# Kernel tuning notes

Measured on AMD Instinct MI355X. Metric: run time of the kernel, lower is better.

## Reference

```python
import jax, jax.numpy as jnp
import numpy as np
from jax import lax

S, B, I, H, L, O, T = 128, 64, 1024, 1024, 2, 1024, 64


def lstm_cell(x, h, c, wih, whh, b):
    # PyTorch gate order: i, f, g, o
    g = x @ wih.T + h @ whh.T + b  # [B, 4H]
    i, f, gg, o = jnp.split(g, 4, axis=-1)
    c = jax.nn.sigmoid(f) * c + jax.nn.sigmoid(i) * jnp.tanh(gg)
    h = jax.nn.sigmoid(o) * jnp.tanh(c)
    return h, c


def run_lstm_seq(xs, wih, whh, b):
    # xs: [S, B, in]; zero initial state (torch default)
    h0 = jnp.zeros((xs.shape[1], whh.shape[-1]), xs.dtype)

    def step(carry, x):
        h, c = lstm_cell(x, carry[0], carry[1], wih, whh, b)
        return (h, c), h

    (h, c), ys = lax.scan(step, (h0, h0), xs)
    return ys, h, c


def setup_inputs() -> dict:
    key = jax.random.key(0)
    ks = jax.random.split(key, 10)
    s = 1.0 / np.sqrt(H)
    u = lambda k, shape: jax.random.uniform(k, shape, minval=-s, maxval=s, dtype=jnp.float32)
    return {
        "input_seq": jax.random.normal(ks[0], (S, B, I), dtype=jnp.float32),
        "enc_wih": u(ks[1], (L, 4 * H, I)),
        "enc_whh": u(ks[2], (L, 4 * H, H)),
        "enc_b": u(ks[3], (L, 4 * H)),
        "dec_wih": u(ks[4], (L, 4 * H, I)),
        "dec_whh": u(ks[5], (L, 4 * H, H)),
        "dec_b": u(ks[6], (L, 4 * H)),
        "lin_w": u(ks[7], (O, H)),
        "lin_b": u(ks[8], (O,)),
        "target_seq_length": T,
    }


def reference(input_seq, enc_wih, enc_whh, enc_b, dec_wih, dec_whh, dec_b, lin_w, lin_b, target_seq_length):
    # ---- encoder: stacked LSTM over the full sequence ----
    xs = input_seq
    hs, cs = [], []
    for l in range(L):
        xs, h, c = run_lstm_seq(xs, enc_wih[l], enc_whh[l], enc_b[l])
        hs.append(h)
        cs.append(c)
    hs = jnp.stack(hs)  # [L, B, H]
    cs = jnp.stack(cs)

    x0 = input_seq[-1]  # [B, I]

    def dec_step(carry, _):
        x, hs, cs = carry
        inp = x
        nh, nc = [], []
        for l in range(L):
            h, c = lstm_cell(inp, hs[l], cs[l], dec_wih[l], dec_whh[l], dec_b[l])
            nh.append(h)
            nc.append(c)
            inp = h
        y = inp @ lin_w.T + lin_b  # [B, O]
        return (y, jnp.stack(nh), jnp.stack(nc)), y

    _, outs = lax.scan(dec_step, (x0, hs, cs), None, length=target_seq_length)
    return jnp.transpose(outs, (1, 0, 2))  # [B, T, O]
```

## Files before the change

### kernel.cpp

```cpp
#include <hip/hip_runtime.h>
#include <math.h>


typedef unsigned short u16;
typedef short short8 __attribute__((ext_vector_type(8)));
typedef float f32x4 __attribute__((ext_vector_type(4)));

#define MFMA_BF16 __builtin_amdgcn_mfma_f32_16x16x32_bf16

__device__ __forceinline__ u16 f2bf(float x) {
  unsigned u = __builtin_bit_cast(unsigned, x);
  unsigned r = u + 0x7fffu + ((u >> 16) & 1u);
  return (u16)(r >> 16);
}
__device__ __forceinline__ float bf2f(u16 b) {
  return __builtin_bit_cast(float, ((unsigned)b) << 16);
}
__device__ __forceinline__ int permrow(int r) {
  int gate = r >> 10, hc = r & 1023;
  return ((hc >> 2) << 4) + ((hc & 3) << 2) + gate;
}

__device__ __forceinline__ void st_sc(u16* p, u16 v) {
  unsigned vv = v;
  asm volatile("global_store_short %0, %1, off sc0 sc1" :: "v"(p), "v"(vv) : "memory");
}
__device__ __forceinline__ int coh_load(const int* p) {
  int v;
  asm volatile("global_load_dword %0, %1, off sc0 sc1\n\ts_waitcnt vmcnt(0)"
               : "=v"(v) : "v"(p) : "memory");
  return v;
}
__device__ __forceinline__ void coh_store(int* p, int v) {
  asm volatile("global_store_dword %0, %1, off sc0 sc1\n\ts_waitcnt vmcnt(0)"
               :: "v"(p), "v"(v) : "memory");
}


__global__ void split_mat(const float* __restrict__ src, u16* __restrict__ dh,
                          u16* __restrict__ dl, int n, int mode) {
  int i = blockIdx.x * 256 + threadIdx.x;
  if (i >= n) return;
  float v = src[i];
  u16 hi = f2bf(v);
  u16 lo = f2bf(v - bf2f(hi));
  int r = i >> 10, c = i & 1023;
  int idx = i;
  if (mode == 1) idx = c * 1024 + r;
  else if (mode == 2) idx = permrow(r) * 1024 + c;
  dh[idx] = hi; dl[idx] = lo;
}

__global__ void zero_f4(float4* __restrict__ p, int n) {
  int i = blockIdx.x * 256 + threadIdx.x;
  if (i < n) p[i] = make_float4(0.f, 0.f, 0.f, 0.f);
}

__global__ void bias_perm(const float* __restrict__ in, float* __restrict__ out) {
  int i = blockIdx.x * 256 + threadIdx.x;
  if (i < 4096) out[permrow(i)] = in[i];
}

__global__ void bias_comb(const float* __restrict__ db0, const float* __restrict__ lb,
                          const float* __restrict__ wih, float* __restrict__ out) {
  __shared__ float red[256];
  int n = blockIdx.x;
  float s = 0.f;
  for (int k = threadIdx.x; k < 1024; k += 256) s += lb[k] * wih[(size_t)n * 1024 + k];
  red[threadIdx.x] = s;
  __syncthreads();
  for (int d = 128; d > 0; d >>= 1) {
    if (threadIdx.x < d) red[threadIdx.x] += red[threadIdx.x + d];
    __syncthreads();
  }
  if (threadIdx.x == 0) out[permrow(n)] = db0[n] + red[0];
}

template<int MT>
__global__ __launch_bounds__(256) void gemm_split(
    const u16* __restrict__ Ah, const u16* __restrict__ Al, int lda,
    const u16* __restrict__ Bh, const u16* __restrict__ Bl, int ldb,
    int K, int gn,
    u16* __restrict__ Ch, u16* __restrict__ Cl, int ldc,
    float* __restrict__ outp, const float* __restrict__ bias, int ldout, int mode) {
  int bm = blockIdx.x / gn, bn = blockIdx.x % gn;
  int l = threadIdx.x & 63, w = threadIdx.x >> 6;
  int n0 = bn * 128 + w * 32;
  int rr = l & 15, ko = (l >> 4) << 3, q = l >> 4;
  int M0 = bm * 64 * MT;
  f32x4 acc[8 * MT] = {};
  for (int kk = 0; kk < K; kk += 32) {
    short8 bh[2], bl[2];
#pragma unroll
    for (int nt = 0; nt < 2; ++nt) {
      size_t bo = (size_t)(n0 + nt * 16 + rr) * ldb + kk + ko;
      bh[nt] = *(const short8*)(Bh + bo);
      bl[nt] = *(const short8*)(Bl + bo);
    }
#pragma unroll
    for (int mt = 0; mt < 4 * MT; ++mt) {
      size_t ao = (size_t)(M0 + mt * 16 + rr) * lda + kk + ko;
      short8 ah = *(const short8*)(Ah + ao);
      short8 al = *(const short8*)(Al + ao);
#pragma unroll
      for (int nt = 0; nt < 2; ++nt) {
        f32x4 t = acc[mt * 2 + nt];
        t = MFMA_BF16(ah, bh[nt], t, 0, 0, 0);
        t = MFMA_BF16(ah, bl[nt], t, 0, 0, 0);
        t = MFMA_BF16(al, bh[nt], t, 0, 0, 0);
        acc[mt * 2 + nt] = t;
      }
    }
  }
#pragma unroll
  for (int mt = 0; mt < 4 * MT; ++mt)
#pragma unroll
    for (int nt = 0; nt < 2; ++nt)
#pragma unroll
      for (int r = 0; r < 4; ++r) {
        int row = M0 + mt * 16 + q * 4 + r;
        int col = n0 + nt * 16 + rr;
        float v = acc[mt * 2 + nt][r];
        if (mode == 0) {
          u16 hh = f2bf(v);
          Ch[(size_t)row * ldc + col] = hh;
          Cl[(size_t)row * ldc + col] = f2bf(v - bf2f(hh));
        } else if (mode == 1) {
          int t = row >> 6, b = row & 63;
          outp[(size_t)b * 65536 + t * 1024 + col] = v + bias[col];
        } else {
          outp[(size_t)row * ldout + col] = v;
        }
      }
}


struct Half {
  const u16 *Ah, *Al, *Wh, *Wl;
  const float* pre;
  const float* bias;
  float* c;
  u16 *Hh, *Hl;
  int active;
};

__global__ __launch_bounds__(512, 1) void lstm_pair(Half hA, Half hB) {
  int j = blockIdx.x;
  Half S = (j < 128) ? hA : hB;
  if (!S.active) return;
  int sub = j & 127;
  int rowblk = ((sub & 7) << 4) | (sub >> 3);
  int R = rowblk << 5;
  int tid = threadIdx.x;
  int l = tid & 63, w = tid >> 6;
  int rr = l & 15, ko = (l >> 4) << 3, q = l >> 4;
  int kb = w << 7;
  const u16* __restrict__ Wh = S.Wh + (size_t)(R + rr) * 1024 + kb + ko;
  const u16* __restrict__ Wl = S.Wl + (size_t)(R + rr) * 1024 + kb + ko;
  const u16* __restrict__ Ah = S.Ah + kb + ko;
  const u16* __restrict__ Al = S.Al + kb + ko;

  f32x4 acc[8] = {};
#pragma unroll
  for (int kk = 0; kk < 128; kk += 32) {
    short8 bh[2], bl[2];
#pragma unroll
    for (int nt = 0; nt < 2; ++nt) {
      bh[nt] = *(const short8*)(Wh + (size_t)(nt << 4) * 1024 + kk);
      bl[nt] = *(const short8*)(Wl + (size_t)(nt << 4) * 1024 + kk);
    }
#pragma unroll
    for (int mt = 0; mt < 4; ++mt) {
      size_t ao = (size_t)((mt << 4) + rr) * 1024 + kk;
      short8 ah = *(const short8*)(Ah + ao);
      short8 al = *(const short8*)(Al + ao);
#pragma unroll
      for (int nt = 0; nt < 2; ++nt) {
        f32x4 t = acc[mt * 2 + nt];
        t = MFMA_BF16(ah, bh[nt], t, 0, 0, 0);
        t = MFMA_BF16(ah, bl[nt], t, 0, 0, 0);
        t = MFMA_BF16(al, bh[nt], t, 0, 0, 0);
        acc[mt * 2 + nt] = t;
      }
    }
  }

  __shared__ float lds[8][64][33];
#pragma unroll
  for (int mt = 0; mt < 4; ++mt)
#pragma unroll
    for (int nt = 0; nt < 2; ++nt)
#pragma unroll
      for (int r = 0; r < 4; ++r)
        lds[w][(mt << 4) + (q << 2) + r][(nt << 4) + rr] = acc[mt * 2 + nt][r];
  __syncthreads();

  int b = tid >> 3, e = tid & 7;
  float g[4];
#pragma unroll
  for (int gt = 0; gt < 4; ++gt) {
    int c = (e << 2) + gt;
    float s = S.bias[R + c] + S.pre[(size_t)b * 4096 + R + c];
#pragma unroll
    for (int ww = 0; ww < 8; ++ww) s += lds[ww][b][c];
    g[gt] = s;
  }
  int hc = (rowblk << 3) + e;
  size_t ci = (size_t)b * 1024 + hc;
  float cold = S.c[ci];
  float is = 1.f / (1.f + expf(-g[0]));
  float fs = 1.f / (1.f + expf(-g[1]));
  float gg = tanhf(g[2]);
  float os = 1.f / (1.f + expf(-g[3]));
  float cn = fs * cold + is * gg;
  S.c[ci] = cn;
  float h = os * tanhf(cn);
  S.Hh[ci] = f2bf(h);
  S.Hl[ci] = f2bf(h - bf2f(f2bf(h)));
}


struct DecP {
  const u16 *Wch, *Wcl;
  const u16 *W0h, *W0l;
  const u16 *Wi1h, *Wi1l;
  const u16 *Wh1h, *Wh1l;
  const u16 *h0i_h, *h0i_l;
  const u16 *h1i_h, *h1i_l;
  const u16 *zh, *zl;
  const float *Gd0, *dbp0, *bdec0, *dbp1;
  const float *c0, *c1;
  u16 *D0h, *D0l;
  u16 *H1h, *H1l;
  int* bar;
};

__device__ __forceinline__ void gridbar(int* arrive, int* go, int seq, int j) {
  __syncthreads();
  int tid = threadIdx.x;
  if (j == 0) {
    if (tid >= 1 && tid < 256) {
      while (coh_load(arrive + tid) < seq) __builtin_amdgcn_s_sleep(1);
    }
    __syncthreads();
    if (tid == 0) coh_store(go, seq);
  } else {
    if (tid == 0) {
      coh_store(arrive + j, seq);
      while (coh_load(go) < seq) __builtin_amdgcn_s_sleep(1);
    }
  }
  __syncthreads();
}

__global__ __launch_bounds__(512, 1) void lstm_dec_persist(DecP D) {
  int j = blockIdx.x;
  int rowblk = ((j & 7) << 5) | (j >> 3);
  int R = rowblk << 4;
  int tid = threadIdx.x;
  int l = tid & 63, w = tid >> 6;
  int rr = l & 15, ko = (l >> 4) << 3, q = l >> 4;
  int opidx = w >> 2;
  int kb = (w & 3) << 8;
  size_t woff = (size_t)(R + rr) * 1024 + kb + ko;
  int* arrive = D.bar;
  int* go = D.bar + 256;

  const u16* pWAh = (opidx == 0 ? D.Wch : D.W0h) + woff;
  const u16* pWAl = (opidx == 0 ? D.Wcl : D.W0l) + woff;
  const u16* pWBh = (opidx == 0 ? D.Wi1h : D.Wh1h) + woff;
  const u16* pWBl = (opidx == 0 ? D.Wi1l : D.Wh1l) + woff;
  short8 wAh[8], wAl[8], wBh[8], wBl[8];
#pragma unroll
  for (int ki = 0; ki < 8; ++ki) {
    wAh[ki] = *(const short8*)(pWAh + (ki << 5));
    wAl[ki] = *(const short8*)(pWAl + (ki << 5));
    wBh[ki] = *(const short8*)(pWBh + (ki << 5));
    wBl[ki] = *(const short8*)(pWBl + (ki << 5));
  }

  float creg0 = 0.f, creg1 = 0.f;
  float bA[4], bB[4], gb0[4];
  size_t ci = 0;
  if (tid < 256) {
    int b = tid >> 2, e = tid & 3;
    int hc = (rowblk << 2) + e;
    ci = (size_t)b * 1024 + hc;
    creg0 = D.c0[ci];
    creg1 = D.c1[ci];
#pragma unroll
    for (int gt = 0; gt < 4; ++gt) {
      int cc = R + (e << 2) + gt;
      bA[gt] = D.bdec0[cc];
      bB[gt] = D.dbp1[cc];
      gb0[gt] = D.dbp0[cc] + D.Gd0[(size_t)(tid >> 2) * 4096 + cc];
    }
  }

  __shared__ float lds[8][64][17];
  const u16 *h0p_h = D.h0i_h, *h0p_l = D.h0i_l;
  int seq = 0;

  for (int t = 0; t < 64; ++t) {
    u16* d0c_h = D.D0h + (size_t)t * 65536;
    u16* d0c_l = D.D0l + (size_t)t * 65536;
    const u16* h1p_h = (t == 0) ? D.h1i_h : D.H1h + (size_t)(t - 1) * 65536;
    const u16* h1p_l = (t == 0) ? D.h1i_l : D.H1l + (size_t)(t - 1) * 65536;

    {
      const u16* Aph = (opidx == 0) ? (t == 0 ? D.zh : h1p_h) : h0p_h;
      const u16* Apl = (opidx == 0) ? (t == 0 ? D.zl : h1p_l) : h0p_l;
      const u16* __restrict__ Ah_ = Aph + kb + ko;
      const u16* __restrict__ Al_ = Apl + kb + ko;
      f32x4 acc[4] = {};
#pragma unroll
      for (int ki = 0; ki < 8; ++ki) {
#pragma unroll
        for (int mt = 0; mt < 4; ++mt) {
          size_t ao = (size_t)((mt << 4) + rr) * 1024 + (ki << 5);
          short8 ah = *(const short8*)(Ah_ + ao);
          short8 al = *(const short8*)(Al_ + ao);
          acc[mt] = MFMA_BF16(ah, wAh[ki], acc[mt], 0, 0, 0);
          acc[mt] = MFMA_BF16(ah, wAl[ki], acc[mt], 0, 0, 0);
          acc[mt] = MFMA_BF16(al, wAh[ki], acc[mt], 0, 0, 0);
        }
      }
#pragma unroll
      for (int mt = 0; mt < 4; ++mt)
#pragma unroll
        for (int r = 0; r < 4; ++r)
          lds[w][(mt << 4) + (q << 2) + r][rr] = acc[mt][r];
    }
    __syncthreads();
    if (tid < 256) {
      int b = tid >> 2, e = tid & 3;
      float g[4];
#pragma unroll
      for (int gt = 0; gt < 4; ++gt) {
        int c = (e << 2) + gt;
        float s = (t == 0) ? gb0[gt] : bA[gt];
#pragma unroll
        for (int ww = 0; ww < 8; ++ww) s += lds[ww][b][c];
        g[gt] = s;
      }
      float is = 1.f / (1.f + expf(-g[0]));
      float fs = 1.f / (1.f + expf(-g[1]));
      float gg = tanhf(g[2]);
      float os = 1.f / (1.f + expf(-g[3]));
      float cn = fs * creg0 + is * gg;
      creg0 = cn;
      float h = os * tanhf(cn);
      u16 hh = f2bf(h);
      st_sc(d0c_h + ci, hh);
      st_sc(d0c_l + ci, f2bf(h - bf2f(hh)));
    }
    gridbar(arrive, go, ++seq, j);

    {
      const u16* Aph = (opidx == 0) ? d0c_h : h1p_h;
      const u16* Apl = (opidx == 0) ? d0c_l : h1p_l;
      const u16* __restrict__ Ah_ = Aph + kb + ko;
      const u16* __restrict__ Al_ = Apl + kb + ko;
      f32x4 acc[4] = {};
#pragma unroll
      for (int ki = 0; ki < 8; ++ki) {
#pragma unroll
        for (int mt = 0; mt < 4; ++mt) {
          size_t ao = (size_t)((mt << 4) + rr) * 1024 + (ki << 5);
          short8 ah = *(const short8*)(Ah_ + ao);
          short8 al = *(const short8*)(Al_ + ao);
          acc[mt] = MFMA_BF16(ah, wBh[ki], acc[mt], 0, 0, 0);
          acc[mt] = MFMA_BF16(ah, wBl[ki], acc[mt], 0, 0, 0);
          acc[mt] = MFMA_BF16(al, wBh[ki], acc[mt], 0, 0, 0);
        }
      }
#pragma unroll
      for (int mt = 0; mt < 4; ++mt)
#pragma unroll
        for (int r = 0; r < 4; ++r)
          lds[w][(mt << 4) + (q << 2) + r][rr] = acc[mt][r];
    }
    __syncthreads();
    if (tid < 256) {
      int b = tid >> 2, e = tid & 3;
      float g[4];
#pragma unroll
      for (int gt = 0; gt < 4; ++gt) {
        int c = (e << 2) + gt;
        float s = bB[gt];
#pragma unroll
        for (int ww = 0; ww < 8; ++ww) s += lds[ww][b][c];
        g[gt] = s;
      }
      float is = 1.f / (1.f + expf(-g[0]));
      float fs = 1.f / (1.f + expf(-g[1]));
      float gg = tanhf(g[2]);
      float os = 1.f / (1.f + expf(-g[3]));
      float cn = fs * creg1 + is * gg;
      creg1 = cn;
      float h = os * tanhf(cn);
      u16 hh = f2bf(h);
      u16 hl = f2bf(h - bf2f(hh));
      size_t hidx = (size_t)t * 65536 + ci;
      st_sc(D.H1h + hidx, hh);
      st_sc(D.H1l + hidx, hl);
    }
    if (t != 63) gridbar(arrive, go, ++seq, j);

    h0p_h = d0c_h; h0p_l = d0c_l;
  }
}


extern "C" void kernel_launch(void* const* d_in, const int* in_sizes, int n_in,
                              void* d_out, int out_size, void* d_ws, size_t ws_size,
                              hipStream_t stream) {
  (void)in_sizes; (void)n_in; (void)out_size; (void)ws_size;
  const float* input_seq = (const float*)d_in[0];
  const float* enc_wih   = (const float*)d_in[1];
  const float* enc_whh   = (const float*)d_in[2];
  const float* enc_b     = (const float*)d_in[3];
  const float* dec_wih   = (const float*)d_in[4];
  const float* dec_whh   = (const float*)d_in[5];
  const float* dec_b     = (const float*)d_in[6];
  const float* lin_w     = (const float*)d_in[7];
  const float* lin_b     = (const float*)d_in[8];
  float* out = (float*)d_out;

  const size_t WE = 4096ull * 1024;
  const size_t HB = 64ull * 1024;
  char* ws = (char*)d_ws;
  size_t off = 0;
  auto alloc16 = [&](size_t elems) {
    u16* p = (u16*)(ws + off);
    off = (off + elems * 2 + 255) & ~(size_t)255;
    return p;
  };
  auto allocf = [&](size_t elems) {
    float* p = (float*)(ws + off);
    off = (off + elems * 4 + 255) & ~(size_t)255;
    return p;
  };

  u16 *WihE0h = alloc16(WE), *WihE0l = alloc16(WE);
  u16 *WhhE0h = alloc16(WE), *WhhE0l = alloc16(WE);
  u16 *WihE1h = alloc16(WE), *WihE1l = alloc16(WE);
  u16 *WhhE1h = alloc16(WE), *WhhE1l = alloc16(WE);
  u16 *WihD0h = alloc16(WE), *WihD0l = alloc16(WE);
  u16 *WhhD0h = alloc16(WE), *WhhD0l = alloc16(WE);
  u16 *WihD1h = alloc16(WE), *WihD1l = alloc16(WE);
  u16 *WhhD1h = alloc16(WE), *WhhD1l = alloc16(WE);
  u16 *Wcombh = alloc16(WE), *Wcombl = alloc16(WE);
  u16 *WLh  = alloc16(1024 * 1024), *WLl  = alloc16(1024 * 1024);
  u16 *WLTh = alloc16(1024 * 1024), *WLTl = alloc16(1024 * 1024);
  u16 *XCh = alloc16(16 * HB), *XCl = alloc16(16 * HB);
  u16 *XLh = alloc16(HB), *XLl = alloc16(HB);
  u16 *H0ch = alloc16(17 * HB), *H0cl = alloc16(17 * HB);
  u16 *H1h = alloc16(64 * HB), *H1l = alloc16(64 * HB);
  u16 *D0h = alloc16(64 * HB), *D0l = alloc16(64 * HB);
  size_t zbeg = off;
  u16 *zh = alloc16(HB), *zl = alloc16(HB);
  float *c0 = allocf(HB), *c1 = allocf(HB);
  int *barbuf = (int*)(ws + off);
  off = (off + 512 * sizeof(int) + 255) & ~(size_t)255;
  size_t zend = off;
  u16 *e1h = alloc16(2 * HB), *e1l = alloc16(2 * HB);
  float *G0 = allocf(1024ull * 4096);
  float *G1 = allocf(1024ull * 4096);
  float *Gd0 = allocf(64 * 4096);
  float *ebp0 = allocf(4096), *ebp1 = allocf(4096);
  float *dbp0 = allocf(4096), *dbp1 = allocf(4096);
  float *bdec0 = allocf(4096);

  {
    int n4 = (int)((zend - zbeg) / 16);
    zero_f4<<<dim3((n4 + 255) / 256), dim3(256), 0, stream>>>((float4*)(ws + zbeg), n4);
  }
  auto split = [&](const float* src, u16* dh, u16* dl, int n, int mode) {
    split_mat<<<dim3((n + 255) / 256), dim3(256), 0, stream>>>(src, dh, dl, n, mode);
  };
  split(enc_wih,        WihE0h, WihE0l, (int)WE, 2);
  split(enc_whh,        WhhE0h, WhhE0l, (int)WE, 2);
  split(enc_wih + WE,   WihE1h, WihE1l, (int)WE, 2);
  split(enc_whh + WE,   WhhE1h, WhhE1l, (int)WE, 2);
  split(dec_wih,        WihD0h, WihD0l, (int)WE, 2);
  split(dec_whh,        WhhD0h, WhhD0l, (int)WE, 2);
  split(dec_wih + WE,   WihD1h, WihD1l, (int)WE, 2);
  split(dec_whh + WE,   WhhD1h, WhhD1l, (int)WE, 2);
  split(lin_w, WLh,  WLl,  1024 * 1024, 0);
  split(lin_w, WLTh, WLTl, 1024 * 1024, 1);
  split(input_seq + 127ull * HB, XLh, XLl, (int)HB, 0);
  bias_perm<<<dim3(16), dim3(256), 0, stream>>>(enc_b,        ebp0);
  bias_perm<<<dim3(16), dim3(256), 0, stream>>>(enc_b + 4096, ebp1);
  bias_perm<<<dim3(16), dim3(256), 0, stream>>>(dec_b,        dbp0);
  bias_perm<<<dim3(16), dim3(256), 0, stream>>>(dec_b + 4096, dbp1);
  bias_comb<<<dim3(4096), dim3(256), 0, stream>>>(dec_b, lin_b, dec_wih, bdec0);
  gemm_split<2><<<dim3(32 * 8), dim3(256), 0, stream>>>(
      WihD0h, WihD0l, 1024, WLTh, WLTl, 1024, 1024, 8,
      Wcombh, Wcombl, 1024, nullptr, nullptr, 0, 0);
  gemm_split<1><<<dim3(32), dim3(256), 0, stream>>>(
      XLh, XLl, 1024, WihD0h, WihD0l, 1024, 1024, 32,
      nullptr, nullptr, 0, Gd0, nullptr, 4096, 2);

  for (int ch = 0; ch < 8; ++ch) {
    split(input_seq + (size_t)ch * 16 * HB, XCh, XCl, (int)(16 * HB), 0);
    gemm_split<2><<<dim3(8 * 32), dim3(256), 0, stream>>>(
        XCh, XCl, 1024, WihE0h, WihE0l, 1024, 1024, 32,
        nullptr, nullptr, 0, G0, nullptr, 4096, 2);
    for (int lt = 0; lt < 16; ++lt) {
      int t0 = ch * 16 + lt;
      int t1 = (ch - 1) * 16 + lt;
      Half A;
      A.Ah = (t0 == 0) ? zh : (lt == 0 ? H0ch + 16ull * HB : H0ch + (size_t)lt * HB);
      A.Al = (t0 == 0) ? zl : (lt == 0 ? H0cl + 16ull * HB : H0cl + (size_t)lt * HB);
      A.Wh = WhhE0h; A.Wl = WhhE0l;
      A.pre = G0 + (size_t)lt * 64 * 4096;
      A.bias = ebp0; A.c = c0;
      A.Hh = H0ch + (size_t)(lt + 1) * HB; A.Hl = H0cl + (size_t)(lt + 1) * HB;
      A.active = 1;
      Half B;
      B.Ah = (t1 == 0) ? zh : e1h + (size_t)((t1 - 1) & 1) * HB;
      B.Al = (t1 == 0) ? zl : e1l + (size_t)((t1 - 1) & 1) * HB;
      B.Wh = WhhE1h; B.Wl = WhhE1l;
      B.pre = G1 + (size_t)lt * 64 * 4096;
      B.bias = ebp1; B.c = c1;
      B.Hh = e1h + (size_t)((t1 >= 0 ? t1 : 0) & 1) * HB;
      B.Hl = e1l + (size_t)((t1 >= 0 ? t1 : 0) & 1) * HB;
      B.active = (ch >= 1) ? 1 : 0;
      lstm_pair<<<dim3(256), dim3(512), 0, stream>>>(A, B);
    }
    gemm_split<2><<<dim3(8 * 32), dim3(256), 0, stream>>>(
        H0ch + HB, H0cl + HB, 1024, WihE1h, WihE1l, 1024, 1024, 32,
        nullptr, nullptr, 0, G1, nullptr, 4096, 2);
  }
  for (int lt = 0; lt < 16; ++lt) {
    int t1 = 112 + lt;
    Half A; A.active = 0;
    A.Ah = zh; A.Al = zl; A.Wh = WhhE0h; A.Wl = WhhE0l;
    A.pre = G0; A.bias = ebp0; A.c = c0; A.Hh = H0ch; A.Hl = H0cl;
    Half B;
    B.Ah = e1h + (size_t)((t1 - 1) & 1) * HB;
    B.Al = e1l + (size_t)((t1 - 1) & 1) * HB;
    B.Wh = WhhE1h; B.Wl = WhhE1l;
    B.pre = G1 + (size_t)lt * 64 * 4096;
    B.bias = ebp1; B.c = c1;
    B.Hh = e1h + (size_t)(t1 & 1) * HB;
    B.Hl = e1l + (size_t)(t1 & 1) * HB;
    B.active = 1;
    lstm_pair<<<dim3(256), dim3(512), 0, stream>>>(A, B);
  }

  {
    DecP P;
    P.Wch = Wcombh; P.Wcl = Wcombl;
    P.W0h = WhhD0h; P.W0l = WhhD0l;
    P.Wi1h = WihD1h; P.Wi1l = WihD1l;
    P.Wh1h = WhhD1h; P.Wh1l = WhhD1l;
    P.h0i_h = H0ch + 16ull * HB; P.h0i_l = H0cl + 16ull * HB;
    P.h1i_h = e1h + HB; P.h1i_l = e1l + HB;
    P.zh = zh; P.zl = zl;
    P.Gd0 = Gd0; P.dbp0 = dbp0; P.bdec0 = bdec0; P.dbp1 = dbp1;
    P.c0 = c0; P.c1 = c1;
    P.D0h = D0h; P.D0l = D0l;
    P.H1h = H1h; P.H1l = H1l;
    P.bar = barbuf;
    lstm_dec_persist<<<dim3(256), dim3(512), 0, stream>>>(P);
  }

  gemm_split<2><<<dim3(32 * 8), dim3(256), 0, stream>>>(
      H1h, H1l, 1024, WLh, WLl, 1024, 1024, 8,
      nullptr, nullptr, 0, out, lin_b, 1024, 1);
}
```

Baseline: 6.493 ms.

## Split decoder layers across block halves with point-to-point flag sync

The persistent decoder kernel previously had all 256 blocks compute layer 0 then layer 1 each step, separated by two full grid barriers. Now blocks 0-127 own layer 0 and blocks 128-255 own layer 1. Each block handles 32 gate rows, holding twice the weights in registers, and syncs via per-block flags. Layer 1 at step t waits only on layer 0's flags for step t, and layer 0 waits on layer 1 for step t-1. This replaces global barriers with producer-consumer flags so the layers can overlap as a pipeline, at the cost of more register pressure and 128 flag polls per step.

```diff
diff --git a/kernel.cpp b/kernel.cpp
--- a/kernel.cpp
+++ b/kernel.cpp
@@ -220,11 +220,11 @@
 }
 
 
-struct DecP {
-  const u16 *Wch, *Wcl;
-  const u16 *W0h, *W0l;
-  const u16 *Wi1h, *Wi1l;
-  const u16 *Wh1h, *Wh1l;
+struct DecL {
+  const u16 *W00h, *W00l;
+  const u16 *W01h, *W01l;
+  const u16 *W10h, *W10l;
+  const u16 *W11h, *W11l;
   const u16 *h0i_h, *h0i_l;
   const u16 *h1i_h, *h1i_l;
   const u16 *zh, *zl;
@@ -235,179 +235,130 @@
   int* bar;
 };
 
-__device__ __forceinline__ void gridbar(int* arrive, int* go, int seq, int j) {
-  __syncthreads();
-  int tid = threadIdx.x;
-  if (j == 0) {
-    if (tid >= 1 && tid < 256) {
-      while (coh_load(arrive + tid) < seq) __builtin_amdgcn_s_sleep(1);
-    }
-    __syncthreads();
-    if (tid == 0) coh_store(go, seq);
-  } else {
-    if (tid == 0) {
-      coh_store(arrive + j, seq);
-      while (coh_load(go) < seq) __builtin_amdgcn_s_sleep(1);
-    }
-  }
-  __syncthreads();
-}
-
-__global__ __launch_bounds__(512, 1) void lstm_dec_persist(DecP D) {
+__global__ __launch_bounds__(512, 1) void lstm_dec_layers(DecL D) {
   int j = blockIdx.x;
-  int rowblk = ((j & 7) << 5) | (j >> 3);
-  int R = rowblk << 4;
+  int lay = j >> 7;
+  int sub = j & 127;
+  int rowblk = ((sub & 7) << 4) | (sub >> 3);
+  int R = rowblk << 5;
   int tid = threadIdx.x;
   int l = tid & 63, w = tid >> 6;
   int rr = l & 15, ko = (l >> 4) << 3, q = l >> 4;
   int opidx = w >> 2;
   int kb = (w & 3) << 8;
-  size_t woff = (size_t)(R + rr) * 1024 + kb + ko;
-  int* arrive = D.bar;
-  int* go = D.bar + 256;
-
-  const u16* pWAh = (opidx == 0 ? D.Wch : D.W0h) + woff;
-  const u16* pWAl = (opidx == 0 ? D.Wcl : D.W0l) + woff;
-  const u16* pWBh = (opidx == 0 ? D.Wi1h : D.Wh1h) + woff;
-  const u16* pWBl = (opidx == 0 ? D.Wi1l : D.Wh1l) + woff;
-  short8 wAh[8], wAl[8], wBh[8], wBl[8];
-#pragma unroll
-  for (int ki = 0; ki < 8; ++ki) {
-    wAh[ki] = *(const short8*)(pWAh + (ki << 5));
-    wAl[ki] = *(const short8*)(pWAl + (ki << 5));
-    wBh[ki] = *(const short8*)(pWBh + (ki << 5));
-    wBl[ki] = *(const short8*)(pWBl + (ki << 5));
-  }
-
-  float creg0 = 0.f, creg1 = 0.f;
-  float bA[4], bB[4], gb0[4];
-  size_t ci = 0;
-  if (tid < 256) {
-    int b = tid >> 2, e = tid & 3;
-    int hc = (rowblk << 2) + e;
-    ci = (size_t)b * 1024 + hc;
-    creg0 = D.c0[ci];
-    creg1 = D.c1[ci];
+  int* flagA = D.bar;
+  int* flagB = D.bar + 2048;
+
+  const u16* Wh_ = lay ? (opidx ? D.W11h : D.W10h) : (opidx ? D.W01h : D.W00h);
+  const u16* Wl_ = lay ? (opidx ? D.W11l : D.W10l) : (opidx ? D.W01l : D.W00l);
+  short8 wh[2][8], wl[2][8];
+#pragma unroll
+  for (int nt = 0; nt < 2; ++nt)
+#pragma unroll
+    for (int ki = 0; ki < 8; ++ki) {
+      size_t o = (size_t)(R + (nt << 4) + rr) * 1024 + kb + (ki << 5) + ko;
+      wh[nt][ki] = *(const short8*)(Wh_ + o);
+      wl[nt][ki] = *(const short8*)(Wl_ + o);
+    }
+
+  int b = tid >> 3, e = tid & 7;
+  int hc = (rowblk << 3) + e;
+  size_t ci = (size_t)b * 1024 + hc;
+  float creg = lay ? D.c1[ci] : D.c0[ci];
+  float bT[4], gb0[4];
+#pragma unroll
+  for (int gt = 0; gt < 4; ++gt) {
+    int cc = R + (e << 2) + gt;
+    bT[gt] = lay ? D.dbp1[cc] : D.bdec0[cc];
+    gb0[gt] = lay ? 0.f : (D.dbp0[cc] + D.Gd0[(size_t)b * 4096 + cc]);
+  }
+
+  __shared__ float lds[8][64][33];
+
+  for (int t = 0; t < 64; ++t) {
+    if (lay) {
+      if (tid < 128) {
+        const int* p = flagA + (tid << 4);
+        while (coh_load(p) < t + 1) __builtin_amdgcn_s_sleep(4);
+      }
+    } else if (t > 0) {
+      if (tid < 128) {
+        const int* p = flagB + (tid << 4);
+        while (coh_load(p) < t) __builtin_amdgcn_s_sleep(4);
+      }
+    }
+    __syncthreads();
+
+    const u16 *Aph, *Apl;
+    if (!lay) {
+      if (opidx == 0) {
+        Aph = t ? D.H1h + (size_t)(t - 1) * 65536 : D.zh;
+        Apl = t ? D.H1l + (size_t)(t - 1) * 65536 : D.zl;
+      } else {
+        Aph = t ? D.D0h + (size_t)(t - 1) * 65536 : D.h0i_h;
+        Apl = t ? D.D0l + (size_t)(t - 1) * 65536 : D.h0i_l;
+      }
+    } else {
+      if (opidx == 0) {
+        Aph = D.D0h + (size_t)t * 65536;
+        Apl = D.D0l + (size_t)t * 65536;
+      } else {
+        Aph = t ? D.H1h + (size_t)(t - 1) * 65536 : D.h1i_h;
+        Apl = t ? D.H1l + (size_t)(t - 1) * 65536 : D.h1i_l;
+      }
+    }
+    const u16* __restrict__ Ah_ = Aph + kb + ko;
+    const u16* __restrict__ Al_ = Apl + kb + ko;
+
+    f32x4 acc[8] = {};
+#pragma unroll
+    for (int ki = 0; ki < 8; ++ki) {
+#pragma unroll
+      for (int mt = 0; mt < 4; ++mt) {
+        size_t ao = (size_t)((mt << 4) + rr) * 1024 + (ki << 5);
+        short8 ah = *(const short8*)(Ah_ + ao);
+        short8 al = *(const short8*)(Al_ + ao);
+#pragma unroll
+        for (int nt = 0; nt < 2; ++nt) {
+          f32x4 tacc = acc[mt * 2 + nt];
+          tacc = MFMA_BF16(ah, wh[nt][ki], tacc, 0, 0, 0);
+          tacc = MFMA_BF16(ah, wl[nt][ki], tacc, 0, 0, 0);
+          tacc = MFMA_BF16(al, wh[nt][ki], tacc, 0, 0, 0);
+          acc[mt * 2 + nt] = tacc;
+        }
+      }
+    }
+#pragma unroll
+    for (int mt = 0; mt < 4; ++mt)
+#pragma unroll
+      for (int nt = 0; nt < 2; ++nt)
+#pragma unroll
+        for (int r = 0; r < 4; ++r)
+          lds[w][(mt << 4) + (q << 2) + r][(nt << 4) + rr] = acc[mt * 2 + nt][r];
+    __syncthreads();
+
+    float g[4];
 #pragma unroll
     for (int gt = 0; gt < 4; ++gt) {
-      int cc = R + (e << 2) + gt;
-      bA[gt] = D.bdec0[cc];
-      bB[gt] = D.dbp1[cc];
-      gb0[gt] = D.dbp0[cc] + D.Gd0[(size_t)(tid >> 2) * 4096 + cc];
-    }
-  }
-
-  __shared__ float lds[8][64][17];
-  const u16 *h0p_h = D.h0i_h, *h0p_l = D.h0i_l;
-  int seq = 0;
-
-  for (int t = 0; t < 64; ++t) {
-    u16* d0c_h = D.D0h + (size_t)t * 65536;
-    u16* d0c_l = D.D0l + (size_t)t * 65536;
-    const u16* h1p_h = (t == 0) ? D.h1i_h : D.H1h + (size_t)(t - 1) * 65536;
-    const u16* h1p_l = (t == 0) ? D.h1i_l : D.H1l + (size_t)(t - 1) * 65536;
-
-    {
-      const u16* Aph = (opidx == 0) ? (t == 0 ? D.zh : h1p_h) : h0p_h;
-      const u16* Apl = (opidx == 0) ? (t == 0 ? D.zl : h1p_l) : h0p_l;
-      const u16* __restrict__ Ah_ = Aph + kb + ko;
-      const u16* __restrict__ Al_ = Apl + kb + ko;
-      f32x4 acc[4] = {};
-#pragma unroll
-      for (int ki = 0; ki < 8; ++ki) {
-#pragma unroll
-        for (int mt = 0; mt < 4; ++mt) {
-          size_t ao = (size_t)((mt << 4) + rr) * 1024 + (ki << 5);
-          short8 ah = *(const short8*)(Ah_ + ao);
-          short8 al = *(const short8*)(Al_ + ao);
-          acc[mt] = MFMA_BF16(ah, wAh[ki], acc[mt], 0, 0, 0);
-          acc[mt] = MFMA_BF16(ah, wAl[ki], acc[mt], 0, 0, 0);
-          acc[mt] = MFMA_BF16(al, wAh[ki], acc[mt], 0, 0, 0);
-        }
-      }
-#pragma unroll
-      for (int mt = 0; mt < 4; ++mt)
-#pragma unroll
-        for (int r = 0; r < 4; ++r)
-          lds[w][(mt << 4) + (q << 2) + r][rr] = acc[mt][r];
-    }
+      int c = (e << 2) + gt;
+      float s = (!lay && t == 0) ? gb0[gt] : bT[gt];
+#pragma unroll
+      for (int ww = 0; ww < 8; ++ww) s += lds[ww][b][c];
+      g[gt] = s;
+    }
+    float is = 1.f / (1.f + expf(-g[0]));
+    float fs = 1.f / (1.f + expf(-g[1]));
+    float gg = tanhf(g[2]);
+    float os = 1.f / (1.f + expf(-g[3]));
+    float cn = fs * creg + is * gg;
+    creg = cn;
+    float h = os * tanhf(cn);
+    u16 hh = f2bf(h), hl = f2bf(h - bf2f(hh));
+    size_t oidx = (size_t)t * 65536 + ci;
+    if (!lay) { st_sc(D.D0h + oidx, hh); st_sc(D.D0l + oidx, hl); }
+    else      { st_sc(D.H1h + oidx, hh); st_sc(D.H1l + oidx, hl); }
     __syncthreads();
-    if (tid < 256) {
-      int b = tid >> 2, e = tid & 3;
-      float g[4];
-#pragma unroll
-      for (int gt = 0; gt < 4; ++gt) {
-        int c = (e << 2) + gt;
-        float s = (t == 0) ? gb0[gt] : bA[gt];
-#pragma unroll
-        for (int ww = 0; ww < 8; ++ww) s += lds[ww][b][c];
-        g[gt] = s;
-      }
-      float is = 1.f / (1.f + expf(-g[0]));
-      float fs = 1.f / (1.f + expf(-g[1]));
-      float gg = tanhf(g[2]);
-      float os = 1.f / (1.f + expf(-g[3]));
-      float cn = fs * creg0 + is * gg;
-      creg0 = cn;
-      float h = os * tanhf(cn);
-      u16 hh = f2bf(h);
-      st_sc(d0c_h + ci, hh);
-      st_sc(d0c_l + ci, f2bf(h - bf2f(hh)));
-    }
-    gridbar(arrive, go, ++seq, j);
-
-    {
-      const u16* Aph = (opidx == 0) ? d0c_h : h1p_h;
-      const u16* Apl = (opidx == 0) ? d0c_l : h1p_l;
-      const u16* __restrict__ Ah_ = Aph + kb + ko;
-      const u16* __restrict__ Al_ = Apl + kb + ko;
-      f32x4 acc[4] = {};
-#pragma unroll
-      for (int ki = 0; ki < 8; ++ki) {
-#pragma unroll
-        for (int mt = 0; mt < 4; ++mt) {
-          size_t ao = (size_t)((mt << 4) + rr) * 1024 + (ki << 5);
-          short8 ah = *(const short8*)(Ah_ + ao);
-          short8 al = *(const short8*)(Al_ + ao);
-          acc[mt] = MFMA_BF16(ah, wBh[ki], acc[mt], 0, 0, 0);
-          acc[mt] = MFMA_BF16(ah, wBl[ki], acc[mt], 0, 0, 0);
-          acc[mt] = MFMA_BF16(al, wBh[ki], acc[mt], 0, 0, 0);
-        }
-      }
-#pragma unroll
-      for (int mt = 0; mt < 4; ++mt)
-#pragma unroll
-        for (int r = 0; r < 4; ++r)
-          lds[w][(mt << 4) + (q << 2) + r][rr] = acc[mt][r];
-    }
-    __syncthreads();
-    if (tid < 256) {
-      int b = tid >> 2, e = tid & 3;
-      float g[4];
-#pragma unroll
-      for (int gt = 0; gt < 4; ++gt) {
-        int c = (e << 2) + gt;
-        float s = bB[gt];
-#pragma unroll
-        for (int ww = 0; ww < 8; ++ww) s += lds[ww][b][c];
-        g[gt] = s;
-      }
-      float is = 1.f / (1.f + expf(-g[0]));
-      float fs = 1.f / (1.f + expf(-g[1]));
-      float gg = tanhf(g[2]);
-      float os = 1.f / (1.f + expf(-g[3]));
-      float cn = fs * creg1 + is * gg;
-      creg1 = cn;
-      float h = os * tanhf(cn);
-      u16 hh = f2bf(h);
-      u16 hl = f2bf(h - bf2f(hh));
-      size_t hidx = (size_t)t * 65536 + ci;
-      st_sc(D.H1h + hidx, hh);
-      st_sc(D.H1l + hidx, hl);
-    }
-    if (t != 63) gridbar(arrive, go, ++seq, j);
-
-    h0p_h = d0c_h; h0p_l = d0c_l;
+    if (tid == 0) coh_store((lay ? flagB : flagA) + (sub << 4), t + 1);
   }
 }
 
@@ -462,7 +413,7 @@
   u16 *zh = alloc16(HB), *zl = alloc16(HB);
   float *c0 = allocf(HB), *c1 = allocf(HB);
   int *barbuf = (int*)(ws + off);
-  off = (off + 512 * sizeof(int) + 255) & ~(size_t)255;
+  off = (off + 4096 * sizeof(int) + 255) & ~(size_t)255;
   size_t zend = off;
   u16 *e1h = alloc16(2 * HB), *e1l = alloc16(2 * HB);
   float *G0 = allocf(1024ull * 4096);
@@ -551,11 +502,11 @@
   }
 
   {
-    DecP P;
-    P.Wch = Wcombh; P.Wcl = Wcombl;
-    P.W0h = WhhD0h; P.W0l = WhhD0l;
-    P.Wi1h = WihD1h; P.Wi1l = WihD1l;
-    P.Wh1h = WhhD1h; P.Wh1l = WhhD1l;
+    DecL P;
+    P.W00h = Wcombh; P.W00l = Wcombl;
+    P.W01h = WhhD0h; P.W01l = WhhD0l;
+    P.W10h = WihD1h; P.W10l = WihD1l;
+    P.W11h = WhhD1h; P.W11l = WhhD1l;
     P.h0i_h = H0ch + 16ull * HB; P.h0i_l = H0cl + 16ull * HB;
     P.h1i_h = e1h + HB; P.h1i_l = e1l + HB;
     P.zh = zh; P.zl = zl;
@@ -564,7 +515,7 @@
     P.D0h = D0h; P.D0l = D0l;
     P.H1h = H1h; P.H1l = H1l;
     P.bar = barbuf;
-    lstm_dec_persist<<<dim3(256), dim3(512), 0, stream>>>(P);
+    lstm_dec_layers<<<dim3(256), dim3(512), 0, stream>>>(P);
   }
 
   gemm_split<2><<<dim3(32 * 8), dim3(256), 0, stream>>>(
```

Result: no change. 6.441 ms (-0.8%).
